# Optimization experiments

Hardware: AMD Instinct MI355X
Metric: run time of the kernel (lower is better)

## Reference

```python
import jax, jax.numpy as jnp
import numpy as np

_EPS = 1e-12      # degenerate-triangle denominator guard
_CHUNK = 64       # triangles processed per scan step


def _bary(p, a, b, c):
    """Barycentric coords of points p w.r.t. triangle (a,b,c). Broadcasts.
    Returns [..., 3] = (u, v, w); -1 everywhere for degenerate triangles."""
    v0 = b - a
    v1 = c - a
    v2 = p - a
    d00 = jnp.sum(v0 * v0, -1)
    d01 = jnp.sum(v0 * v1, -1)
    d11 = jnp.sum(v1 * v1, -1)
    d20 = jnp.sum(v2 * v0, -1)
    d21 = jnp.sum(v2 * v1, -1)
    denom = d00 * d11 - d01 * d01
    bad = jnp.abs(denom) < _EPS
    ds = jnp.where(bad, 1.0, denom)
    v = (d11 * d20 - d01 * d21) / ds
    w = (d00 * d21 - d01 * d20) / ds
    u = 1.0 - v - w
    bar = jnp.stack([u, v, w], -1)
    return jnp.where(bad[..., None], -1.0, bar)


def _pixel_grid(res):
    # pixel-center UVs; x = u along columns, y = v along rows
    t = (jnp.arange(res, dtype=jnp.float32) + 0.5) / res
    gy, gx = jnp.meshgrid(t, t, indexing='ij')
    return jnp.stack([gx, gy], -1)  # [res, res, 2]


def _rasterize_ids(uv, face_indices, res):
    """For each bake pixel, the index of the first (lowest-index) triangle
    containing it, or -1 (== rast[...,-1] in the slang kernel)."""
    px = _pixel_grid(res)                    # [H, W, 2]
    tri = uv[face_indices]                   # [Nf, 3, 2]
    nf = tri.shape[0]
    nchunk = nf // _CHUNK
    tri_c = tri[: nchunk * _CHUNK].reshape(nchunk, _CHUNK, 3, 2)
    fid0 = jnp.full((res, res), -1, dtype=jnp.int32)

    def step(fid, xs):
        ci, tc = xs                          # tc: [C, 3, 2]
        bar = _bary(px[:, :, None, :], tc[:, 0], tc[:, 1], tc[:, 2])  # [H, W, C, 3]
        inside = jnp.all(bar >= 0.0, axis=-1)                          # [H, W, C]
        hit = jnp.any(inside, axis=-1)
        first = jnp.argmax(inside, axis=-1).astype(jnp.int32)          # first hit in chunk
        cand = ci * _CHUNK + first
        fid = jnp.where(hit & (fid < 0), cand, fid)
        return fid, None

    fid, _ = jax.lax.scan(step, fid0, (jnp.arange(nchunk, dtype=jnp.int32), tri_c))
    return fid


def _interpolate(attr, uv, face_indices, fid, res):
    px = _pixel_grid(res)
    tri_idx = face_indices[jnp.clip(fid, 0)]        # [H, W, 3] vertex ids of hit face
    verts = uv[tri_idx]                             # [H, W, 3, 2]
    bar = _bary(px, verts[..., 0, :], verts[..., 1, :], verts[..., 2, :])  # [H, W, 3]
    av = attr[tri_idx]                              # [H, W, 3, 3]
    out = jnp.einsum('hwk,hwkc->hwc', bar, av)
    return jnp.where(fid[..., None] >= 0, out, 0.0)  # zeros outside coverage (kernel inits output to 0)


def setup_inputs() -> dict:
    key = jax.random.key(0)
    k1, k2, k3 = jax.random.split(key, 3)
    Nv, Nf, res = 50000, 512, 512
    attr = jax.random.normal(k1, (Nv, 3), dtype=jnp.float32)
    uv = jax.random.uniform(k2, (Nv, 2), dtype=jnp.float32)
    face_indices = jax.random.randint(k3, (Nf, 3), 0, Nv, dtype=jnp.int32)
    return {"attr": attr, "uv": uv, "face_indices": face_indices, "bake_resolution": res}


def reference(attr, uv, face_indices, bake_resolution):
    fid = _rasterize_ids(uv, face_indices, bake_resolution)
    return _interpolate(attr, uv, face_indices, fid, bake_resolution)
```

## Files before the change

kernel.cpp:

```cpp
#include <hip/hip_runtime.h>
#include <math.h>

#pragma clang fp contract(off)

#define TB_NT 512
#define TS    16

__device__ inline float bcast(float x, int l) {
    return __int_as_float(__builtin_amdgcn_readlane(__float_as_int(x), l));
}

__global__ void tb_setup(const float* __restrict__ uv,
                         const int*   __restrict__ fidx,
                         float4* __restrict__ R0, float4* __restrict__ R1,
                         float2* __restrict__ R2, float4* __restrict__ BB,
                         int n_used) {
    int t = blockIdx.x * blockDim.x + threadIdx.x;
    if (t >= n_used) return;
    int i0 = fidx[3 * t + 0];
    int i1 = fidx[3 * t + 1];
    int i2 = fidx[3 * t + 2];
    float ax = uv[2 * i0], ay = uv[2 * i0 + 1];
    float bx = uv[2 * i1], by = uv[2 * i1 + 1];
    float cx = uv[2 * i2], cy = uv[2 * i2 + 1];
    float v0x = bx - ax, v0y = by - ay;
    float v1x = cx - ax, v1y = cy - ay;
    float d00 = v0x * v0x + v0y * v0y;
    float d01 = v0x * v1x + v0y * v1y;
    float d11 = v1x * v1x + v1y * v1y;
    float denom = d00 * d11 - d01 * d01;
    float ds = (fabsf(denom) < 1e-12f) ? 0.0f : denom;
    R0[t] = make_float4(ax, ay, v0x, v0y);
    R1[t] = make_float4(v1x, v1y, d01, ds);
    R2[t] = make_float2(d11, d00);
    if (ds == 0.0f) {
        BB[t] = make_float4(2.0f, -1.0f, 2.0f, -1.0f);
    } else {
        BB[t] = make_float4(fminf(ax, fminf(bx, cx)),
                            fmaxf(ax, fmaxf(bx, cx)),
                            fminf(ay, fminf(by, cy)),
                            fmaxf(ay, fmaxf(by, cy)));
    }
}

__global__ __launch_bounds__(256)
void tb_bake(const float*  __restrict__ attr,
             const int*    __restrict__ fidx,
             const float4* __restrict__ R0, const float4* __restrict__ R1,
             const float2* __restrict__ R2, const float4* __restrict__ BB,
             float* __restrict__ out,
             int res, int n_used, int tiles_x) {
    int bx = blockIdx.x % tiles_x;
    int by = blockIdx.x / tiles_x;
    int tx = threadIdx.x & (TS - 1);
    int ty = threadIdx.x >> 4;
    int w = bx * TS + tx;
    int h = by * TS + ty;
    bool live = (w < res) && (h < res);
    int pix = h * res + w;
    float pxx = ((float)w + 0.5f) / (float)res;
    float pxy = ((float)h + 0.5f) / (float)res;

    int wv = threadIdx.x >> 6;
    int ln = threadIdx.x & 63;

    float wx0 = (float)(bx * TS) / (float)res;
    float wx1 = (float)(bx * TS + TS) / (float)res;
    float wy0 = (float)(by * TS + wv * 4) / (float)res;
    float wy1 = (float)(by * TS + wv * 4 + 4) / (float)res;

    int   hit = -1;
    float bu = 0.0f, bv = 0.0f, bw = 0.0f;

    int nslab = n_used >> 6;

    float4 cbb = BB[ln];
    float4 cr0 = R0[ln];
    float4 cr1 = R1[ln];
    float2 cr2 = R2[ln];

    for (int s = 0; s < nslab; ++s) {
        float4 nbb = make_float4(2.0f, -1.0f, 2.0f, -1.0f);
        float4 nr0 = cr0, nr1 = cr1;
        float2 nr2 = cr2;
        if (s + 1 < nslab) {
            int tn = (s + 1) * 64 + ln;
            nbb = BB[tn];
            nr0 = R0[tn];
            nr1 = R1[tn];
            nr2 = R2[tn];
        }

        bool p = (cbb.y >= wx0) && (cbb.x <= wx1) &&
                 (cbb.w >= wy0) && (cbb.z <= wy1);
        unsigned long long mask = __ballot((int)p);

        while (mask) {
            int l = (int)__ffsll(mask) - 1;
            mask &= (mask - 1);
            float ax  = bcast(cr0.x, l);
            float ay  = bcast(cr0.y, l);
            float v0x = bcast(cr0.z, l);
            float v0y = bcast(cr0.w, l);
            float v1x = bcast(cr1.x, l);
            float v1y = bcast(cr1.y, l);
            float d01 = bcast(cr1.z, l);
            float ds  = bcast(cr1.w, l);
            float d11 = bcast(cr2.x, l);
            float d00 = bcast(cr2.y, l);
            float v2x = pxx - ax;
            float v2y = pxy - ay;
            float d20 = v2x * v0x + v2y * v0y;
            float d21 = v2x * v1x + v2y * v1y;
            float vn = d11 * d20 - d01 * d21;
            float wn = d00 * d21 - d01 * d20;
            float sg = (ds > 0.0f) ? 1.0f : -1.0f;
            if (hit < 0 && vn * sg >= 0.0f && wn * sg >= 0.0f) {
                float v  = vn / ds;
                float ww = wn / ds;
                float u  = (1.0f - v) - ww;
                if (u >= 0.0f) {
                    bu = u; bv = v; bw = ww;
                    hit = s * 64 + l;
                }
            }
            if (__all((int)(hit >= 0 || !live))) break;
        }
        if (__all((int)(hit >= 0 || !live))) break;

        cbb = nbb; cr0 = nr0; cr1 = nr1; cr2 = nr2;
    }

    if (live) {
        float o0 = 0.0f, o1 = 0.0f, o2 = 0.0f;
        if (hit >= 0) {
            int i0 = fidx[3 * hit + 0];
            int i1 = fidx[3 * hit + 1];
            int i2 = fidx[3 * hit + 2];
            o0 = (bu * attr[3 * i0 + 0] + bv * attr[3 * i1 + 0]) + bw * attr[3 * i2 + 0];
            o1 = (bu * attr[3 * i0 + 1] + bv * attr[3 * i1 + 1]) + bw * attr[3 * i2 + 1];
            o2 = (bu * attr[3 * i0 + 2] + bv * attr[3 * i1 + 2]) + bw * attr[3 * i2 + 2];
        }
        out[3 * pix + 0] = o0;
        out[3 * pix + 1] = o1;
        out[3 * pix + 2] = o2;
    }
}

extern "C" void kernel_launch(void* const* d_in, const int* in_sizes, int n_in,
                              void* d_out, int out_size, void* d_ws, size_t ws_size,
                              hipStream_t stream) {
    const float* attr = (const float*)d_in[0];
    const float* uv   = (const float*)d_in[1];
    const int*   fidx = (const int*)d_in[2];
    float*       out  = (float*)d_out;

    int res = (int)lround(sqrt((double)(out_size / 3)));
    int nf = in_sizes[2] / 3;
    int n_used = (nf / 64) * 64;

    float4* R0 = (float4*)d_ws;
    float4* R1 = R0 + TB_NT;
    float2* R2 = (float2*)(R1 + TB_NT);
    float4* BB = (float4*)(R2 + TB_NT);

    if (n_used > 0) {
        tb_setup<<<(n_used + 255) / 256, 256, 0, stream>>>(uv, fidx, R0, R1, R2, BB, n_used);
    }
    int tiles_x = (res + TS - 1) / TS;
    int nblocks = tiles_x * tiles_x;
    tb_bake<<<nblocks, 256, 0, stream>>>(attr, fidx, R0, R1, R2, BB,
                                         out, res, n_used, tiles_x);
}
```

Measured before the change: 79.33 us.

## Fuse triangle setup into bake kernel and interpolate attributes at hit time

Removes the separate tb_setup kernel launch. Each wave now gathers face indices and UVs and computes triangle setup values and bounding boxes itself, slab by slab. The attribute interpolation moves into the hit path, using face indices broadcast across lanes, so the final fidx reload is no longer needed. The trade-off is that every one of the 1024 blocks redundantly recomputes setup for all triangles, with dependent gather loads, to save one launch and the workspace round-trip.

```diff
diff --git a/kernel.cpp b/kernel.cpp
--- a/kernel.cpp
+++ b/kernel.cpp
@@ -3,53 +3,23 @@
 
 #pragma clang fp contract(off)
 
-#define TB_NT 512
-#define TS    16
+#define TS 16
 
-__device__ inline float bcast(float x, int l) {
+__device__ inline float bcastf(float x, int l) {
     return __int_as_float(__builtin_amdgcn_readlane(__float_as_int(x), l));
 }
-
-__global__ void tb_setup(const float* __restrict__ uv,
-                         const int*   __restrict__ fidx,
-                         float4* __restrict__ R0, float4* __restrict__ R1,
-                         float2* __restrict__ R2, float4* __restrict__ BB,
-                         int n_used) {
-    int t = blockIdx.x * blockDim.x + threadIdx.x;
-    if (t >= n_used) return;
-    int i0 = fidx[3 * t + 0];
-    int i1 = fidx[3 * t + 1];
-    int i2 = fidx[3 * t + 2];
-    float ax = uv[2 * i0], ay = uv[2 * i0 + 1];
-    float bx = uv[2 * i1], by = uv[2 * i1 + 1];
-    float cx = uv[2 * i2], cy = uv[2 * i2 + 1];
-    float v0x = bx - ax, v0y = by - ay;
-    float v1x = cx - ax, v1y = cy - ay;
-    float d00 = v0x * v0x + v0y * v0y;
-    float d01 = v0x * v1x + v0y * v1y;
-    float d11 = v1x * v1x + v1y * v1y;
-    float denom = d00 * d11 - d01 * d01;
-    float ds = (fabsf(denom) < 1e-12f) ? 0.0f : denom;
-    R0[t] = make_float4(ax, ay, v0x, v0y);
-    R1[t] = make_float4(v1x, v1y, d01, ds);
-    R2[t] = make_float2(d11, d00);
-    if (ds == 0.0f) {
-        BB[t] = make_float4(2.0f, -1.0f, 2.0f, -1.0f);
-    } else {
-        BB[t] = make_float4(fminf(ax, fminf(bx, cx)),
-                            fmaxf(ax, fmaxf(bx, cx)),
-                            fminf(ay, fminf(by, cy)),
-                            fmaxf(ay, fmaxf(by, cy)));
-    }
+__device__ inline int bcasti(int x, int l) {
+    return __builtin_amdgcn_readlane(x, l);
 }
 
 __global__ __launch_bounds__(256)
-void tb_bake(const float*  __restrict__ attr,
-             const int*    __restrict__ fidx,
-             const float4* __restrict__ R0, const float4* __restrict__ R1,
-             const float2* __restrict__ R2, const float4* __restrict__ BB,
-             float* __restrict__ out,
+void tb_bake(const float* __restrict__ attr,
+             const float* __restrict__ uv,
+             const int*   __restrict__ fidx,
+             float*       __restrict__ out,
              int res, int n_used, int tiles_x) {
+    const float2* uv2 = (const float2*)uv;
+
     int bx = blockIdx.x % tiles_x;
     int by = blockIdx.x / tiles_x;
     int tx = threadIdx.x & (TS - 1);
@@ -70,77 +40,94 @@
     float wy1 = (float)(by * TS + wv * 4 + 4) / (float)res;
 
     int   hit = -1;
-    float bu = 0.0f, bv = 0.0f, bw = 0.0f;
+    float o0 = 0.0f, o1 = 0.0f, o2 = 0.0f;
 
     int nslab = n_used >> 6;
 
-    float4 cbb = BB[ln];
-    float4 cr0 = R0[ln];
-    float4 cr1 = R1[ln];
-    float2 cr2 = R2[ln];
+    int ci0 = 0, ci1 = 0, ci2 = 0;
+    float2 cpa = make_float2(0.f, 0.f), cpb = cpa, cpc = cpa;
+    if (nslab > 0) {
+        ci0 = fidx[3 * ln + 0];
+        ci1 = fidx[3 * ln + 1];
+        ci2 = fidx[3 * ln + 2];
+        cpa = uv2[ci0];
+        cpb = uv2[ci1];
+        cpc = uv2[ci2];
+    }
 
     for (int s = 0; s < nslab; ++s) {
-        float4 nbb = make_float4(2.0f, -1.0f, 2.0f, -1.0f);
-        float4 nr0 = cr0, nr1 = cr1;
-        float2 nr2 = cr2;
+        int ni0 = ci0, ni1 = ci1, ni2 = ci2;
+        float2 npa = cpa, npb = cpb, npc = cpc;
         if (s + 1 < nslab) {
             int tn = (s + 1) * 64 + ln;
-            nbb = BB[tn];
-            nr0 = R0[tn];
-            nr1 = R1[tn];
-            nr2 = R2[tn];
+            ni0 = fidx[3 * tn + 0];
+            ni1 = fidx[3 * tn + 1];
+            ni2 = fidx[3 * tn + 2];
+            npa = uv2[ni0];
+            npb = uv2[ni1];
+            npc = uv2[ni2];
         }
 
-        bool p = (cbb.y >= wx0) && (cbb.x <= wx1) &&
-                 (cbb.w >= wy0) && (cbb.z <= wy1);
+        float ax = cpa.x, ay = cpa.y;
+        float v0x = cpb.x - ax, v0y = cpb.y - ay;
+        float v1x = cpc.x - ax, v1y = cpc.y - ay;
+        float d00 = v0x * v0x + v0y * v0y;
+        float d01 = v0x * v1x + v0y * v1y;
+        float d11 = v1x * v1x + v1y * v1y;
+        float denom = d00 * d11 - d01 * d01;
+        float ds = (fabsf(denom) < 1e-12f) ? 0.0f : denom;
+        float mnx = fminf(ax, fminf(cpb.x, cpc.x));
+        float mxx = fmaxf(ax, fmaxf(cpb.x, cpc.x));
+        float mny = fminf(ay, fminf(cpb.y, cpc.y));
+        float mxy = fmaxf(ay, fmaxf(cpb.y, cpc.y));
+        bool p = (ds != 0.0f) &&
+                 (mxx >= wx0) && (mnx <= wx1) &&
+                 (mxy >= wy0) && (mny <= wy1);
         unsigned long long mask = __ballot((int)p);
 
         while (mask) {
             int l = (int)__ffsll(mask) - 1;
             mask &= (mask - 1);
-            float ax  = bcast(cr0.x, l);
-            float ay  = bcast(cr0.y, l);
-            float v0x = bcast(cr0.z, l);
-            float v0y = bcast(cr0.w, l);
-            float v1x = bcast(cr1.x, l);
-            float v1y = bcast(cr1.y, l);
-            float d01 = bcast(cr1.z, l);
-            float ds  = bcast(cr1.w, l);
-            float d11 = bcast(cr2.x, l);
-            float d00 = bcast(cr2.y, l);
-            float v2x = pxx - ax;
-            float v2y = pxy - ay;
-            float d20 = v2x * v0x + v2y * v0y;
-            float d21 = v2x * v1x + v2y * v1y;
-            float vn = d11 * d20 - d01 * d21;
-            float wn = d00 * d21 - d01 * d20;
-            float sg = (ds > 0.0f) ? 1.0f : -1.0f;
+            float bax  = bcastf(ax,  l);
+            float bay  = bcastf(ay,  l);
+            float bv0x = bcastf(v0x, l);
+            float bv0y = bcastf(v0y, l);
+            float bv1x = bcastf(v1x, l);
+            float bv1y = bcastf(v1y, l);
+            float bd01 = bcastf(d01, l);
+            float bds  = bcastf(ds,  l);
+            float bd11 = bcastf(d11, l);
+            float bd00 = bcastf(d00, l);
+            float v2x = pxx - bax;
+            float v2y = pxy - bay;
+            float d20 = v2x * bv0x + v2y * bv0y;
+            float d21 = v2x * bv1x + v2y * bv1y;
+            float vn = bd11 * d20 - bd01 * d21;
+            float wn = bd00 * d21 - bd01 * d20;
+            float sg = (bds > 0.0f) ? 1.0f : -1.0f;
             if (hit < 0 && vn * sg >= 0.0f && wn * sg >= 0.0f) {
-                float v  = vn / ds;
-                float ww = wn / ds;
+                float v  = vn / bds;
+                float ww = wn / bds;
                 float u  = (1.0f - v) - ww;
                 if (u >= 0.0f) {
-                    bu = u; bv = v; bw = ww;
                     hit = s * 64 + l;
+                    int j0 = bcasti(ci0, l);
+                    int j1 = bcasti(ci1, l);
+                    int j2 = bcasti(ci2, l);
+                    o0 = (u * attr[3 * j0 + 0] + v * attr[3 * j1 + 0]) + ww * attr[3 * j2 + 0];
+                    o1 = (u * attr[3 * j0 + 1] + v * attr[3 * j1 + 1]) + ww * attr[3 * j2 + 1];
+                    o2 = (u * attr[3 * j0 + 2] + v * attr[3 * j1 + 2]) + ww * attr[3 * j2 + 2];
                 }
             }
             if (__all((int)(hit >= 0 || !live))) break;
         }
         if (__all((int)(hit >= 0 || !live))) break;
 
-        cbb = nbb; cr0 = nr0; cr1 = nr1; cr2 = nr2;
+        ci0 = ni0; ci1 = ni1; ci2 = ni2;
+        cpa = npa; cpb = npb; cpc = npc;
     }
 
     if (live) {
-        float o0 = 0.0f, o1 = 0.0f, o2 = 0.0f;
-        if (hit >= 0) {
-            int i0 = fidx[3 * hit + 0];
-            int i1 = fidx[3 * hit + 1];
-            int i2 = fidx[3 * hit + 2];
-            o0 = (bu * attr[3 * i0 + 0] + bv * attr[3 * i1 + 0]) + bw * attr[3 * i2 + 0];
-            o1 = (bu * attr[3 * i0 + 1] + bv * attr[3 * i1 + 1]) + bw * attr[3 * i2 + 1];
-            o2 = (bu * attr[3 * i0 + 2] + bv * attr[3 * i1 + 2]) + bw * attr[3 * i2 + 2];
-        }
         out[3 * pix + 0] = o0;
         out[3 * pix + 1] = o1;
         out[3 * pix + 2] = o2;
@@ -159,16 +146,7 @@
     int nf = in_sizes[2] / 3;
     int n_used = (nf / 64) * 64;
 
-    float4* R0 = (float4*)d_ws;
-    float4* R1 = R0 + TB_NT;
-    float2* R2 = (float2*)(R1 + TB_NT);
-    float4* BB = (float4*)(R2 + TB_NT);
-
-    if (n_used > 0) {
-        tb_setup<<<(n_used + 255) / 256, 256, 0, stream>>>(uv, fidx, R0, R1, R2, BB, n_used);
-    }
     int tiles_x = (res + TS - 1) / TS;
     int nblocks = tiles_x * tiles_x;
-    tb_bake<<<nblocks, 256, 0, stream>>>(attr, fidx, R0, R1, R2, BB,
-                                         out, res, n_used, tiles_x);
+    tb_bake<<<nblocks, 256, 0, stream>>>(attr, uv, fidx, out, res, n_used, tiles_x);
 }
```

New measurement: 79.47 us. About the same (+0.2%).
